# Kernel optimization log

Hardware: AMD Instinct MI355X
Metric: run time of the kernel (lower is better)

## Reference

```python
import jax, jax.numpy as jnp
import numpy as np

N_NODES = 100000
N_EDGES = 262144
IN_DIM = 768
HIDDEN = 256


def setup_inputs() -> dict:
    key = jax.random.key(0)
    ks = jax.random.split(key, 8)
    x_src = jax.random.normal(ks[0], (N_NODES, IN_DIM), dtype=jnp.float32)
    x_dst = jax.random.normal(ks[1], (N_NODES, IN_DIM), dtype=jnp.float32)
    s_idx = jax.random.randint(ks[2], (N_EDGES,), 0, N_NODES, dtype=jnp.int32)
    d_idx = jax.random.randint(ks[3], (N_EDGES,), 0, N_NODES, dtype=jnp.int32)
    # MLP params: Linear(2*in_dim -> hidden), Linear(hidden -> 1)
    lim1 = 1.0 / np.sqrt(2 * IN_DIM)
    W1 = jax.random.uniform(ks[4], (2 * IN_DIM, HIDDEN), minval=-lim1, maxval=lim1, dtype=jnp.float32)
    b1 = jax.random.uniform(ks[5], (HIDDEN,), minval=-lim1, maxval=lim1, dtype=jnp.float32)
    lim2 = 1.0 / np.sqrt(HIDDEN)
    W2 = jax.random.uniform(ks[6], (HIDDEN, 1), minval=-lim2, maxval=lim2, dtype=jnp.float32)
    b2 = jax.random.uniform(ks[7], (1,), minval=-lim2, maxval=lim2, dtype=jnp.float32)
    return {"x_src": x_src, "x_dst": x_dst, "s_idx": s_idx, "d_idx": d_idx,
            "W1": W1, "b1": b1, "W2": W2, "b2": b2}


def reference(x_src, x_dst, s_idx, d_idx, W1, b1, W2, b2):
    # h = concat([x_src[s], x_dst[d]], axis=1) @ W1 + b1
    # Expressed without materializing the [E, 2*in_dim] concat by splitting W1.
    h = (jnp.take(x_src, s_idx, axis=0) @ W1[:IN_DIM]
         + jnp.take(x_dst, d_idx, axis=0) @ W1[IN_DIM:]
         + b1)  # [E, hidden]
    h = jax.nn.relu(h)  # dropout is identity in eval mode
    logits = h @ W2 + b2  # [E, 1]
    return logits.reshape(-1)
```

## Files before the change

kernel.cpp:

```cpp
#include <hip/hip_runtime.h>
#include <hip/hip_bf16.h>

#define N_NODES 100000
#define N_EDGES 262144
#define IN_DIM 768
#define HIDDEN 256
#define BM 128
#define BN 256
#define BK 32
#define NK (IN_DIM / BK)
#define M_BLOCKS 782
#define M_PAD (M_BLOCKS * BM)
#define WT_TILE_BYTES (BN * BK * 2)

typedef __attribute__((ext_vector_type(8))) short short8;
typedef __attribute__((ext_vector_type(4))) float f32x4;

#define WAITV(n) asm volatile("s_waitcnt vmcnt(" #n ")" ::: "memory")
#define FENCE()  asm volatile("" ::: "memory")

__device__ __forceinline__ unsigned short f32_to_bf16(float f) {
    unsigned int u = __builtin_bit_cast(unsigned int, f);
    u = (u + 0x7FFFu + ((u >> 16) & 1u)) >> 16;
    return (unsigned short)u;
}
__device__ __forceinline__ float bf16_to_f32(unsigned short h) {
    unsigned int u = ((unsigned int)h) << 16;
    return __builtin_bit_cast(float, u);
}
__device__ __forceinline__ void gload_lds16(const void* gsrc, void* lds) {
    __builtin_amdgcn_global_load_lds(
        (const __attribute__((address_space(1))) unsigned int*)gsrc,
        (__attribute__((address_space(3))) unsigned int*)lds,
        16, 0, 0);
}

__global__ __launch_bounds__(256) void convert_w1(const float* __restrict__ W1,
                                                  unsigned short* __restrict__ WtT) {
    int t = blockIdx.x * blockDim.x + threadIdx.x;
    if (t >= 2 * NK * BN * BK) return;
    int g  = t / (NK * BN * BK);
    int r  = t % (NK * BN * BK);
    int ks = r / (BN * BK);
    int r2 = r % (BN * BK);
    int s  = r2 >> 3;
    int j  = r2 & 7;
    int n  = s >> 2;
    int p  = s & 3;
    int k  = ks * BK + ((p ^ ((n >> 1) & 3)) << 3) + j;
    WtT[t] = f32_to_bf16(W1[(size_t)(g * IN_DIM + k) * HIDDEN + n]);
}

__global__ __launch_bounds__(512, 4) void node_gemm(const float* __restrict__ X0,
                                                    const float* __restrict__ X1,
                                                    const unsigned short* __restrict__ WtT,
                                                    unsigned short* __restrict__ Pout,
                                                    unsigned short* __restrict__ Qout) {
    const int g = blockIdx.y;
    const float* __restrict__ X = g ? X1 : X0;
    unsigned short* __restrict__ Out = g ? Qout : Pout;
    const char* wt_base = (const char*)WtT + (size_t)g * NK * WT_TILE_BYTES;

    __shared__ __attribute__((aligned(16))) char As[2][BM * BK * 4];
    __shared__ __attribute__((aligned(16))) char Bs[2][BN * BK * 2];

    const int m0   = blockIdx.x * BM;
    const int tid  = threadIdx.x;
    const int lane = tid & 63;
    const int wid  = tid >> 6;
    const int wm   = wid >> 2;
    const int wn   = wid & 3;

    f32x4 acc[4][4] = {};

    const int a_row_in_inst = lane >> 3;
    const int a_perm        = ((lane & 7) ^ a_row_in_inst) << 2;

    auto issue = [&](int ks, int buf) {
        const int k0 = ks * BK;
#pragma unroll
        for (int j = 0; j < 2; ++j) {
            int r  = (wid * 2 + j) * 8 + a_row_in_inst;
            int rg = m0 + r;
            if (rg >= N_NODES) rg = N_NODES - 1;
            gload_lds16(X + (size_t)rg * IN_DIM + k0 + a_perm,
                        As[buf] + (wid * 2 + j) * 1024);
        }
        const char* src = wt_base + (size_t)ks * WT_TILE_BYTES + (wid * 2) * 1024 + lane * 16;
#pragma unroll
        for (int j = 0; j < 2; ++j)
            gload_lds16(src + j * 1024, Bs[buf] + (wid * 2 + j) * 1024);
    };

    auto compute = [&](int buf) {
        const char* ab = As[buf];
        const char* bb = Bs[buf];
        const int lr = lane & 15;
        const int c  = lane >> 4;
        short8 bfr[4];
#pragma unroll
        for (int ni = 0; ni < 4; ++ni) {
            int n = wn * 64 + ni * 16 + lr;
            bfr[ni] = *(const short8*)(bb + n * 64 + ((c ^ ((n >> 1) & 3)) << 4));
        }
        __builtin_amdgcn_s_setprio(1);
#pragma unroll
        for (int mi = 0; mi < 4; ++mi) {
            int r = wm * 64 + mi * 16 + lr;
            const char* rowp = ab + r * 128;
            float4 lo = *(const float4*)(rowp + (((2 * c)     ^ (r & 7)) << 4));
            float4 hi = *(const float4*)(rowp + (((2 * c + 1) ^ (r & 7)) << 4));
            short8 a;
            a[0] = f32_to_bf16(lo.x); a[1] = f32_to_bf16(lo.y);
            a[2] = f32_to_bf16(lo.z); a[3] = f32_to_bf16(lo.w);
            a[4] = f32_to_bf16(hi.x); a[5] = f32_to_bf16(hi.y);
            a[6] = f32_to_bf16(hi.z); a[7] = f32_to_bf16(hi.w);
#pragma unroll
            for (int ni = 0; ni < 4; ++ni)
                acc[mi][ni] = __builtin_amdgcn_mfma_f32_16x16x32_bf16(
                    bfr[ni], a, acc[mi][ni], 0, 0, 0);
        }
        __builtin_amdgcn_s_setprio(0);
    };

    issue(0, 0);
    issue(1, 1);
    WAITV(4);
    __builtin_amdgcn_s_barrier();
    FENCE();

    for (int ks = 0; ks < NK; ++ks) {
        const int buf = ks & 1;
        compute(buf);
        FENCE();
        __builtin_amdgcn_s_barrier();
        FENCE();
        if (ks + 2 < NK) {
            issue(ks + 2, buf);
            WAITV(4);
        } else {
            WAITV(0);
        }
        __builtin_amdgcn_s_barrier();
        FENCE();
    }

    const int mrow = wm * 64 + (lane & 15);
    const int nb0  = wn * 64 + ((lane >> 4) << 2);
#pragma unroll
    for (int mi = 0; mi < 4; ++mi) {
        size_t mg = (size_t)(m0 + mrow + mi * 16);
#pragma unroll
        for (int ni = 0; ni < 4; ++ni) {
            f32x4 a = acc[mi][ni];
            ushort4 w;
            w.x = f32_to_bf16(a[0]); w.y = f32_to_bf16(a[1]);
            w.z = f32_to_bf16(a[2]); w.w = f32_to_bf16(a[3]);
            *(ushort4*)(Out + mg * HIDDEN + nb0 + ni * 16) = w;
        }
    }
}

__global__ __launch_bounds__(256) void edge_mlp(const unsigned short* __restrict__ P,
                                                const unsigned short* __restrict__ Q,
                                                const int* __restrict__ s_idx,
                                                const int* __restrict__ d_idx,
                                                const float* __restrict__ b1,
                                                const float* __restrict__ W2,
                                                const float* __restrict__ b2,
                                                float* __restrict__ out) {
    const int lane = threadIdx.x & 63;
    const int gw = (blockIdx.x * blockDim.x + threadIdx.x) >> 6;
    const int nw = (gridDim.x * blockDim.x) >> 6;
    const float4 b1v = *(const float4*)(b1 + lane * 4);
    const float4 w2v = *(const float4*)(W2 + lane * 4);
    const float b2s = *b2;
    for (int e = gw; e < N_EDGES; e += nw) {
        int s = s_idx[e];
        int d = d_idx[e];
        ushort4 pv = *(const ushort4*)(P + (size_t)s * HIDDEN + lane * 4);
        ushort4 qv = *(const ushort4*)(Q + (size_t)d * HIDDEN + lane * 4);
        float h, sum;
        h = bf16_to_f32(pv.x) + bf16_to_f32(qv.x) + b1v.x; h = fmaxf(h, 0.f); sum  = h * w2v.x;
        h = bf16_to_f32(pv.y) + bf16_to_f32(qv.y) + b1v.y; h = fmaxf(h, 0.f); sum += h * w2v.y;
        h = bf16_to_f32(pv.z) + bf16_to_f32(qv.z) + b1v.z; h = fmaxf(h, 0.f); sum += h * w2v.z;
        h = bf16_to_f32(pv.w) + bf16_to_f32(qv.w) + b1v.w; h = fmaxf(h, 0.f); sum += h * w2v.w;
#pragma unroll
        for (int off = 32; off; off >>= 1) sum += __shfl_xor(sum, off, 64);
        if (lane == 0) out[e] = sum + b2s;
    }
}

extern "C" void kernel_launch(void* const* d_in, const int* in_sizes, int n_in,
                              void* d_out, int out_size, void* d_ws, size_t ws_size,
                              hipStream_t stream) {
    const float* x_src = (const float*)d_in[0];
    const float* x_dst = (const float*)d_in[1];
    const int*   s_idx = (const int*)d_in[2];
    const int*   d_idx = (const int*)d_in[3];
    const float* W1    = (const float*)d_in[4];
    const float* b1    = (const float*)d_in[5];
    const float* W2    = (const float*)d_in[6];
    const float* b2    = (const float*)d_in[7];
    float* out = (float*)d_out;

    char* ws = (char*)d_ws;
    unsigned short* WtT = (unsigned short*)ws;
    unsigned short* P   = (unsigned short*)(ws + 786432);
    unsigned short* Q   = (unsigned short*)(ws + 786432 + (size_t)M_PAD * HIDDEN * 2);

    convert_w1<<<(2 * NK * BN * BK + 255) / 256, 256, 0, stream>>>(W1, WtT);

    dim3 gg(M_BLOCKS, 2);
    node_gemm<<<gg, 512, 0, stream>>>(x_src, x_dst, WtT, P, Q);

    edge_mlp<<<2048, 256, 0, stream>>>(P, Q, s_idx, d_idx, b1, W2, b2, out);
}
```

Before: 251.5 us.

## Stage A tile through registers with bf16 conversion and triple-buffered LDS pipeline

```diff
diff --git a/kernel.cpp b/kernel.cpp
--- a/kernel.cpp
+++ b/kernel.cpp
@@ -17,6 +17,7 @@
 typedef __attribute__((ext_vector_type(4))) float f32x4;
 
 #define WAITV(n) asm volatile("s_waitcnt vmcnt(" #n ")" ::: "memory")
+#define WAITL()  asm volatile("s_waitcnt lgkmcnt(0)" ::: "memory")
 #define FENCE()  asm volatile("" ::: "memory")
 
 __device__ __forceinline__ unsigned short f32_to_bf16(float f) {
@@ -61,8 +62,8 @@
     unsigned short* __restrict__ Out = g ? Qout : Pout;
     const char* wt_base = (const char*)WtT + (size_t)g * NK * WT_TILE_BYTES;
 
-    __shared__ __attribute__((aligned(16))) char As[2][BM * BK * 4];
-    __shared__ __attribute__((aligned(16))) char Bs[2][BN * BK * 2];
+    __shared__ __attribute__((aligned(16))) char As[3][BM * BK * 2];
+    __shared__ __attribute__((aligned(16))) char Bs[3][BN * BK * 2];
 
     const int m0   = blockIdx.x * BM;
     const int tid  = threadIdx.x;
@@ -71,82 +72,96 @@
     const int wm   = wid >> 2;
     const int wn   = wid & 3;
 
+    const int sr = tid >> 2;
+    const int sc = tid & 3;
+    int srow_g = m0 + sr;
+    if (srow_g >= N_NODES) srow_g = N_NODES - 1;
+    const float* aptr = X + (size_t)srow_g * IN_DIM + sc * 8;
+    const int awoff = sr * 64 + (((sc ^ ((sr >> 1) & 3))) << 4);
+
     f32x4 acc[4][4] = {};
-
-    const int a_row_in_inst = lane >> 3;
-    const int a_perm        = ((lane & 7) ^ a_row_in_inst) << 2;
-
-    auto issue = [&](int ks, int buf) {
-        const int k0 = ks * BK;
-#pragma unroll
-        for (int j = 0; j < 2; ++j) {
-            int r  = (wid * 2 + j) * 8 + a_row_in_inst;
-            int rg = m0 + r;
-            if (rg >= N_NODES) rg = N_NODES - 1;
-            gload_lds16(X + (size_t)rg * IN_DIM + k0 + a_perm,
-                        As[buf] + (wid * 2 + j) * 1024);
+    float4 bank0[2], bank1[2];
+
+    auto a_issue = [&](int ks, float4 (&bk)[2]) {
+        const float* p = aptr + ks * BK;
+        bk[0] = *(const float4*)(p);
+        bk[1] = *(const float4*)(p + 4);
+    };
+    auto a_write = [&](int slot, const float4 (&bk)[2]) {
+        short8 w;
+        w[0] = (short)f32_to_bf16(bk[0].x); w[1] = (short)f32_to_bf16(bk[0].y);
+        w[2] = (short)f32_to_bf16(bk[0].z); w[3] = (short)f32_to_bf16(bk[0].w);
+        w[4] = (short)f32_to_bf16(bk[1].x); w[5] = (short)f32_to_bf16(bk[1].y);
+        w[6] = (short)f32_to_bf16(bk[1].z); w[7] = (short)f32_to_bf16(bk[1].w);
+        *(short8*)(As[slot] + awoff) = w;
+    };
+    auto b_issue = [&](int ks, int slot) {
+        const char* src = wt_base + (size_t)ks * WT_TILE_BYTES + wid * 2048 + lane * 16;
+        char* dst = Bs[slot] + wid * 2048;
+        gload_lds16(src, dst);
+        gload_lds16(src + 1024, dst + 1024);
+    };
+
+    const int lr = lane & 15;
+    const int c  = lane >> 4;
+
+    auto step = [&](int ks, float4 (&bk)[2]) {
+        const char* Ab = As[ks % 3];
+        const char* Bb = Bs[ks % 3];
+        short8 afr[4], bfr[4];
+#pragma unroll
+        for (int mi = 0; mi < 4; ++mi) {
+            int r = wm * 64 + mi * 16 + lr;
+            afr[mi] = *(const short8*)(Ab + r * 64 + ((c ^ ((r >> 1) & 3)) << 4));
         }
-        const char* src = wt_base + (size_t)ks * WT_TILE_BYTES + (wid * 2) * 1024 + lane * 16;
-#pragma unroll
-        for (int j = 0; j < 2; ++j)
-            gload_lds16(src + j * 1024, Bs[buf] + (wid * 2 + j) * 1024);
-    };
-
-    auto compute = [&](int buf) {
-        const char* ab = As[buf];
-        const char* bb = Bs[buf];
-        const int lr = lane & 15;
-        const int c  = lane >> 4;
-        short8 bfr[4];
 #pragma unroll
         for (int ni = 0; ni < 4; ++ni) {
             int n = wn * 64 + ni * 16 + lr;
-            bfr[ni] = *(const short8*)(bb + n * 64 + ((c ^ ((n >> 1) & 3)) << 4));
+            bfr[ni] = *(const short8*)(Bb + n * 64 + ((c ^ ((n >> 1) & 3)) << 4));
         }
         __builtin_amdgcn_s_setprio(1);
 #pragma unroll
-        for (int mi = 0; mi < 4; ++mi) {
-            int r = wm * 64 + mi * 16 + lr;
-            const char* rowp = ab + r * 128;
-            float4 lo = *(const float4*)(rowp + (((2 * c)     ^ (r & 7)) << 4));
-            float4 hi = *(const float4*)(rowp + (((2 * c + 1) ^ (r & 7)) << 4));
-            short8 a;
-            a[0] = f32_to_bf16(lo.x); a[1] = f32_to_bf16(lo.y);
-            a[2] = f32_to_bf16(lo.z); a[3] = f32_to_bf16(lo.w);
-            a[4] = f32_to_bf16(hi.x); a[5] = f32_to_bf16(hi.y);
-            a[6] = f32_to_bf16(hi.z); a[7] = f32_to_bf16(hi.w);
+        for (int mi = 0; mi < 4; ++mi)
 #pragma unroll
             for (int ni = 0; ni < 4; ++ni)
                 acc[mi][ni] = __builtin_amdgcn_mfma_f32_16x16x32_bf16(
-                    bfr[ni], a, acc[mi][ni], 0, 0, 0);
-        }
+                    bfr[ni], afr[mi], acc[mi][ni], 0, 0, 0);
         __builtin_amdgcn_s_setprio(0);
-    };
-
-    issue(0, 0);
-    issue(1, 1);
-    WAITV(4);
-    __builtin_amdgcn_s_barrier();
-    FENCE();
-
-    for (int ks = 0; ks < NK; ++ks) {
-        const int buf = ks & 1;
-        compute(buf);
+        const int wslot = (ks + 2) % 3;
+        const int kB = (ks + 2 < NK) ? ks + 2 : NK - 1;
+        b_issue(kB, wslot);
+        WAITV(4);
+        a_write(wslot, bk);
+        const int kA = (ks + 4 < NK) ? ks + 4 : NK - 1;
+        a_issue(kA, bk);
         FENCE();
         __builtin_amdgcn_s_barrier();
         FENCE();
-        if (ks + 2 < NK) {
-            issue(ks + 2, buf);
-            WAITV(4);
-        } else {
-            WAITV(0);
-        }
-        __builtin_amdgcn_s_barrier();
-        FENCE();
+    };
+
+    a_issue(0, bank0);
+    a_issue(1, bank1);
+    b_issue(0, 0);
+    WAITV(4);
+    a_write(0, bank0);
+    a_issue(2, bank0);
+    WAITV(4);
+    a_write(1, bank1);
+    b_issue(1, 1);
+    a_issue(3, bank1);
+    WAITV(6);
+    WAITL();
+    FENCE();
+    __builtin_amdgcn_s_barrier();
+    FENCE();
+
+    for (int ks2 = 0; ks2 < NK; ks2 += 2) {
+        step(ks2, bank0);
+        step(ks2 + 1, bank1);
     }
 
-    const int mrow = wm * 64 + (lane & 15);
-    const int nb0  = wn * 64 + ((lane >> 4) << 2);
+    const int mrow = wm * 64 + lr;
+    const int nb0  = wn * 64 + (c << 2);
 #pragma unroll
     for (int mi = 0; mi < 4; ++mi) {
         size_t mg = (size_t)(m0 + mrow + mi * 16);
@@ -159,6 +174,7 @@
             *(ushort4*)(Out + mg * HIDDEN + nb0 + ni * 16) = w;
         }
     }
+    WAITV(0);
 }
 
 __global__ __launch_bounds__(256) void edge_mlp(const unsigned short* __restrict__ P,
```

Measured after the change: 239.3 us. -4.8%, faster.
